# Optimization experiments

Measured on AMD Instinct MI355X. Metric: run time of the kernel, lower is better.

The kernel has to match this reference:

```python
import jax, jax.numpy as jnp
import numpy as np
from jax import lax

RADIUS = 0.3
NSAMPLE = 16
NPOINT = 1024
NH = 1   # num_heading_bin
NS = 18  # num_size_cluster
EPS = 1e-5  # torch BatchNorm eps


def _bn(x, g, b, m, v):
    # eval-mode batchnorm over the last (channel) axis
    return (x - m) * (g / jnp.sqrt(v + EPS)) + b


def _fps(xyz, npoint):
    # furthest point sampling; xyz: (B,K,3) -> (B,npoint) int32 indices
    B, K, _ = xyz.shape
    def body(carry, _):
        dists, far = carry
        cur = jnp.take_along_axis(xyz, far[:, None, None], axis=1)  # (B,1,3)
        d = jnp.sum((xyz - cur) ** 2, -1)                           # (B,K)
        dists = jnp.minimum(dists, d)
        nxt = jnp.argmax(dists, -1).astype(jnp.int32)
        return (dists, nxt), far
    init = (jnp.full((B, K), 1e10, xyz.dtype), jnp.zeros((B,), jnp.int32))
    _, inds = lax.scan(body, init, None, length=npoint)
    return jnp.swapaxes(inds, 0, 1)  # (B, npoint)


def _ball_query(xyz, new_xyz):
    # first-NSAMPLE points within RADIUS of each center, pad with first hit
    K = xyz.shape[1]
    d2 = jnp.sum((new_xyz[:, :, None, :] - xyz[:, None, :, :]) ** 2, -1)  # (B,S,K)
    mask = d2 < RADIUS ** 2
    idx = jnp.where(mask, jnp.arange(K, dtype=jnp.int32)[None, None, :], K)
    idx = jnp.sort(idx, -1)[..., :NSAMPLE]
    first = idx[..., :1]
    idx = jnp.where(idx == K, first, idx)
    idx = jnp.where(idx == K, 0, idx)  # degenerate: no neighbor at all
    return idx  # (B,S,NSAMPLE)


def setup_inputs() -> dict:
    key = jax.random.key(0)
    ks = jax.random.split(key, 32)
    inp = {}
    inp['xyz'] = jax.random.normal(ks[0], (8, 8192, 3), jnp.float32)
    inp['features'] = jax.random.normal(ks[1], (8, 256, 8192), jnp.float32)
    i = 2
    # shared MLP: 259 -> 128 -> 128 -> 128 (conv2d 1x1, no bias, then BN)
    for l, (o, c) in enumerate([(128, 259), (128, 128), (128, 128)]):
        inp[f'mlp_w{l}'] = jax.random.normal(ks[i], (o, c), jnp.float32) * 0.1; i += 1
        inp[f'mlp_g{l}'] = jnp.ones((o,), jnp.float32)
        inp[f'mlp_b{l}'] = jnp.zeros((o,), jnp.float32)
        inp[f'mlp_m{l}'] = jax.random.normal(ks[i], (o,), jnp.float32) * 0.01; i += 1
        inp[f'mlp_v{l}'] = jax.random.uniform(ks[i], (o,), jnp.float32, 0.5, 1.5); i += 1
    # box head convs (conv1d k=1)
    for nm, (o, c) in [('c1', (128, 128)), ('c2', (128, 128)), ('c3', (97, 128))]:
        inp[f'{nm}_w'] = jax.random.normal(ks[i], (o, c), jnp.float32) * 0.1; i += 1
        inp[f'{nm}_b'] = jnp.zeros((o,), jnp.float32)
    for nm in ['bn1', 'bn2']:
        inp[f'{nm}_g'] = jnp.ones((128,), jnp.float32)
        inp[f'{nm}_b'] = jnp.zeros((128,), jnp.float32)
        inp[f'{nm}_m'] = jax.random.normal(ks[i], (128,), jnp.float32) * 0.01; i += 1
        inp[f'{nm}_v'] = jax.random.uniform(ks[i], (128,), jnp.float32, 0.5, 1.5); i += 1
    inp['mean_size_arr'] = jax.random.uniform(ks[i], (NS, 3), jnp.float32, 0.3, 2.0)
    return inp


def reference(xyz, features,
              mlp_w0, mlp_g0, mlp_b0, mlp_m0, mlp_v0,
              mlp_w1, mlp_g1, mlp_b1, mlp_m1, mlp_v1,
              mlp_w2, mlp_g2, mlp_b2, mlp_m2, mlp_v2,
              c1_w, c1_b, bn1_g, bn1_b, bn1_m, bn1_v,
              c2_w, c2_b, bn2_g, bn2_b, bn2_m, bn2_v,
              c3_w, c3_b, mean_size_arr):
    B = xyz.shape[0]
    # --- vote aggregation: FPS + ball query + group + shared MLP + maxpool ---
    fps_inds = _fps(xyz, NPOINT)
    new_xyz = jnp.take_along_axis(xyz, fps_inds[..., None], axis=1)  # (B,S,3)
    idx = _ball_query(xyz, new_xyz)                                  # (B,S,n)
    gather = jax.vmap(lambda a, i: a[i])
    g_xyz = (gather(xyz, idx) - new_xyz[:, :, None, :]) / RADIUS     # normalize_xyz
    g_f = gather(jnp.swapaxes(features, 1, 2), idx)                  # (B,S,n,256)
    h = jnp.concatenate([g_xyz, g_f], -1)                            # (B,S,n,259)
    for w, g, b, m, v in ((mlp_w0, mlp_g0, mlp_b0, mlp_m0, mlp_v0),
                          (mlp_w1, mlp_g1, mlp_b1, mlp_m1, mlp_v1),
                          (mlp_w2, mlp_g2, mlp_b2, mlp_m2, mlp_v2)):
        h = jax.nn.relu(_bn(jnp.einsum('bsnc,oc->bsno', h, w), g, b, m, v))
    feat = jnp.max(h, axis=2)                                        # (B,S,128)
    # --- box head (conv1d k=1 == per-point linear) ---
    net = jax.nn.relu(_bn(jnp.einsum('bsc,oc->bso', feat, c1_w) + c1_b,
                          bn1_g, bn1_b, bn1_m, bn1_v))
    net = jax.nn.relu(_bn(jnp.einsum('bsc,oc->bso', net, c2_w) + c2_b,
                          bn2_g, bn2_b, bn2_m, bn2_v))
    net = jnp.einsum('bsc,oc->bso', net, c3_w) + c3_b                # (B,S,97)
    # --- decode_scores ---
    obj = net[..., 0:2]
    center = new_xyz + net[..., 2:5]
    hs = net[..., 5:5 + NH]
    hr = net[..., 5 + NH:5 + 2 * NH] * (np.pi / NH)
    ss = net[..., 5 + 2 * NH:5 + 2 * NH + NS]
    srn = net[..., 5 + 2 * NH + NS:5 + 2 * NH + 4 * NS].reshape(B, NPOINT, NS, 3)
    sr = (srn * mean_size_arr[None, None]).reshape(B, NPOINT, NS * 3)
    sem = net[..., 5 + 2 * NH + 4 * NS:]
    return jnp.concatenate([obj, center, hs, hr, ss, sr, sem], -1)   # (B,S,97)
```

## Files before the change

### kernel.cpp

```cpp
#include <hip/hip_runtime.h>
#include <cstdint>
#include <cstddef>

#define BATCH   8
#define KPTS    8192
#define NPT     1024
#define NSAMP   16
#define RAD2    0.09f

typedef float f32x2 __attribute__((ext_vector_type(2)));
typedef float f32x4 __attribute__((ext_vector_type(4)));
typedef short s16x4 __attribute__((ext_vector_type(4)));
typedef short s16x8 __attribute__((ext_vector_type(8)));

__device__ __forceinline__ unsigned short f2bf(float x) {
    unsigned u = __float_as_uint(x);
    return (unsigned short)((u + 0x7fffu + ((u >> 16) & 1u)) >> 16);
}

template <int CTRL>
__device__ __forceinline__ unsigned long long dpp_max_step(unsigned long long v) {
    unsigned int lo = (unsigned int)v, hi = (unsigned int)(v >> 32);
    unsigned int lo2 = (unsigned int)__builtin_amdgcn_update_dpp(0, (int)lo, CTRL, 0xf, 0xf, true);
    unsigned int hi2 = (unsigned int)__builtin_amdgcn_update_dpp(0, (int)hi, CTRL, 0xf, 0xf, true);
    unsigned long long o = ((unsigned long long)hi2 << 32) | lo2;
    return o > v ? o : v;
}

__global__ __launch_bounds__(512, 1) void fps_f0_kernel(
    const float* __restrict__ xyz, float* __restrict__ new_xyz,
    const float* __restrict__ feats, const float* __restrict__ w0,
    float* __restrict__ f0out) {
    __shared__ float xs[KPTS], ys[KPTS], zs[KPTS];
    __shared__ __align__(16) unsigned long long wslot[2][8];
    __shared__ int   hist[NPT];
    __shared__ float As[16 * 128];
    __shared__ float Bs[16 * 130];

    const int tid = threadIdx.x;

    if (blockIdx.x >= 8) {
        const int bid = blockIdx.x - 8;
        const int b   = bid >> 6;
        const int p0  = (bid & 63) << 7;
        const int rb  = (tid >> 4) << 2;
        const int ob  = tid & 15;
        const float* fb = feats + (size_t)b * 256 * KPTS;

        float acc[4][8];
#pragma unroll
        for (int r = 0; r < 4; ++r)
#pragma unroll
            for (int c = 0; c < 8; ++c) acc[r][c] = 0.f;

        for (int k0 = 0; k0 < 256; k0 += 16) {
#pragma unroll
            for (int i = 0; i < 4; ++i) {
                int e = tid + (i << 9);
                int kk = e >> 7, pc = e & 127;
                As[kk * 128 + pc] = fb[(size_t)(k0 + kk) * KPTS + p0 + pc];
            }
#pragma unroll
            for (int i = 0; i < 4; ++i) {
                int e = tid + (i << 9);
                int o = e >> 4, kk = e & 15;
                Bs[kk * 130 + o] = w0[o * 259 + 3 + k0 + kk];
            }
            __syncthreads();
#pragma unroll
            for (int kk = 0; kk < 16; ++kk) {
                float a[4], wvv[8];
#pragma unroll
                for (int r = 0; r < 4; ++r) a[r] = As[kk * 128 + rb + r];
#pragma unroll
                for (int c = 0; c < 8; ++c) wvv[c] = Bs[kk * 130 + ob + (c << 4)];
#pragma unroll
                for (int r = 0; r < 4; ++r)
#pragma unroll
                    for (int c = 0; c < 8; ++c) acc[r][c] = fmaf(a[r], wvv[c], acc[r][c]);
            }
            __syncthreads();
        }
#pragma unroll
        for (int r = 0; r < 4; ++r) {
            float* outp = f0out + ((size_t)b * KPTS + p0 + rb + r) * 128 + ob;
#pragma unroll
            for (int c = 0; c < 8; ++c) outp[c << 4] = acc[r][c];
        }
        return;
    }

    {
#pragma clang fp contract(off)
        const int b = blockIdx.x;
        const float* xb = xyz + (size_t)b * KPTS * 3;

        for (int i = tid; i < KPTS; i += 512) {
            xs[i] = xb[i * 3 + 0];
            ys[i] = xb[i * 3 + 1];
            zs[i] = xb[i * 3 + 2];
        }
        __syncthreads();

        const int base = tid << 4;
        f32x2 px[8], py[8], pz[8], dmn[8];
#pragma unroll
        for (int j = 0; j < 8; ++j) {
            int i0 = base + (j << 1);
            px[j] = (f32x2){xs[i0], xs[i0 + 1]};
            py[j] = (f32x2){ys[i0], ys[i0 + 1]};
            pz[j] = (f32x2){zs[i0], zs[i0 + 1]};
            dmn[j] = (f32x2){1e10f, 1e10f};
        }

        int far = 0;
        for (int it = 0; it < NPT; ++it) {
            if (tid == 0) hist[it] = far;
            const float cx = xs[far], cy = ys[far], cz = zs[far];
            const f32x2 cx2 = (f32x2){cx, cx};
            const f32x2 cy2 = (f32x2){cy, cy};
            const f32x2 cz2 = (f32x2){cz, cz};

            f32x2 mm = (f32x2){-1.0f, -1.0f};
#pragma unroll
            for (int j = 0; j < 8; ++j) {
                f32x2 dx = px[j] - cx2;
                f32x2 dy = py[j] - cy2;
                f32x2 dz = pz[j] - cz2;
                f32x2 d  = (dx * dx + dy * dy) + dz * dz;
                f32x2 nd = __builtin_elementwise_min(dmn[j], d);
                dmn[j] = nd;
                mm = __builtin_elementwise_max(mm, nd);
            }
            float lmax = fmaxf(mm.x, mm.y);

            int ci = 0x7fffffff;
#pragma unroll
            for (int j = 0; j < 8; ++j) {
                if (dmn[j].x == lmax) ci = min(ci, base + (j << 1));
                if (dmn[j].y == lmax) ci = min(ci, base + (j << 1) + 1);
            }

            unsigned long long pk =
                ((unsigned long long)__float_as_uint(lmax) << 32) | (unsigned)(8191 - ci);

            pk = dpp_max_step<0x111>(pk);
            pk = dpp_max_step<0x112>(pk);
            pk = dpp_max_step<0x114>(pk);
            pk = dpp_max_step<0x118>(pk);
            pk = dpp_max_step<0x142>(pk);
            pk = dpp_max_step<0x143>(pk);

            if ((tid & 63) == 63) wslot[it & 1][tid >> 6] = pk;
            __syncthreads();

            ulonglong2 s01 = *(const ulonglong2*)&wslot[it & 1][0];
            ulonglong2 s23 = *(const ulonglong2*)&wslot[it & 1][2];
            ulonglong2 s45 = *(const ulonglong2*)&wslot[it & 1][4];
            ulonglong2 s67 = *(const ulonglong2*)&wslot[it & 1][6];
            unsigned long long g = s01.x;
            if (s01.y > g) g = s01.y;
            if (s23.x > g) g = s23.x;
            if (s23.y > g) g = s23.y;
            if (s45.x > g) g = s45.x;
            if (s45.y > g) g = s45.y;
            if (s67.x > g) g = s67.x;
            if (s67.y > g) g = s67.y;
            far = 8191 - (int)(unsigned)(g & 0xffffffffull);
        }

        for (int i = tid; i < NPT; i += 512) {
            int idx = hist[i];
            float* o = new_xyz + ((size_t)b * NPT + i) * 3;
            o[0] = xs[idx]; o[1] = ys[idx]; o[2] = zs[idx];
        }
    }
}

__global__ __launch_bounds__(256) void ballq_kernel(const float* __restrict__ xyz,
                                                    const float* __restrict__ new_xyz,
                                                    int* __restrict__ idxout) {
    const int tid  = threadIdx.x;
    const int lane = tid & 63;
    const int q    = (blockIdx.x << 2) + (tid >> 6);
    const int b    = q >> 10;
    const float* xb = xyz + (size_t)b * KPTS * 3;
    const float qx = new_xyz[q * 3 + 0];
    const float qy = new_xyz[q * 3 + 1];
    const float qz = new_xyz[q * 3 + 2];
    int* op = idxout + q * NSAMP;

    int total = 0;
    int first_p = 0;
    for (int c = 0; c < KPTS / 64; ++c) {
        int p = (c << 6) + lane;
        float pxv = xb[p * 3 + 0], pyv = xb[p * 3 + 1], pzv = xb[p * 3 + 2];
        float dx = __fsub_rn(qx, pxv), dy = __fsub_rn(qy, pyv), dz = __fsub_rn(qz, pzv);
        float d2 = __fadd_rn(__fadd_rn(__fmul_rn(dx, dx), __fmul_rn(dy, dy)),
                             __fmul_rn(dz, dz));
        bool pred = d2 < RAD2;
        unsigned long long mask = __ballot(pred);
        if (total == 0 && mask != 0ull) first_p = (c << 6) + (int)__builtin_ctzll(mask);
        if (pred) {
            int rank = (int)__popcll(mask & ((1ull << lane) - 1ull));
            int slot = total + rank;
            if (slot < NSAMP) op[slot] = p;
        }
        total += (int)__popcll(mask);
        if (total >= NSAMP) break;
    }
    if (total < NSAMP && lane >= total && lane < NSAMP) op[lane] = first_p;
}

#define HB 136

__global__ __launch_bounds__(256) void mlp_kernel(
    const float* __restrict__ f0, const int* __restrict__ idxw,
    const float* __restrict__ xyz, const float* __restrict__ new_xyz,
    const float* __restrict__ w0,
    const float* __restrict__ g0, const float* __restrict__ b0,
    const float* __restrict__ m0, const float* __restrict__ v0,
    const float* __restrict__ w1,
    const float* __restrict__ g1, const float* __restrict__ b1a,
    const float* __restrict__ m1, const float* __restrict__ v1,
    const float* __restrict__ w2,
    const float* __restrict__ g2, const float* __restrict__ b2a,
    const float* __restrict__ m2, const float* __restrict__ v2,
    float* __restrict__ featout) {
    const int tid = threadIdx.x;
    const int q0  = blockIdx.x << 2;
    const int b   = q0 >> 10;

    __shared__ __align__(16) unsigned short hbf[64 * HB];
    __shared__ __align__(16) unsigned short Wsh[128 * HB];
    __shared__ float gx[64], gy[64], gz[64];
    __shared__ int   pidx[64];
    __shared__ float s0[128], t0[128], wxs[128], wys[128], wzs[128];
    __shared__ float s1[128], t1[128], s2[128], t2[128];

    if (tid < 64) pidx[tid] = idxw[(q0 + (tid >> 4)) * NSAMP + (tid & 15)];
    if (tid < 128) {
        float sc = g0[tid] / sqrtf(v0[tid] + 1e-5f);
        s0[tid] = sc; t0[tid] = b0[tid] - m0[tid] * sc;
        sc = g1[tid] / sqrtf(v1[tid] + 1e-5f);
        s1[tid] = sc; t1[tid] = b1a[tid] - m1[tid] * sc;
        sc = g2[tid] / sqrtf(v2[tid] + 1e-5f);
        s2[tid] = sc; t2[tid] = b2a[tid] - m2[tid] * sc;
        wxs[tid] = w0[tid * 259 + 0];
        wys[tid] = w0[tid * 259 + 1];
        wzs[tid] = w0[tid * 259 + 2];
    }
    __syncthreads();
    if (tid < 64) {
        int p = pidx[tid];
        int q = q0 + (tid >> 4);
        const float* pp = xyz + ((size_t)b * KPTS + p) * 3;
        const float* nq = new_xyz + (size_t)q * 3;
        gx[tid] = (pp[0] - nq[0]) / 0.3f;
        gy[tid] = (pp[1] - nq[1]) / 0.3f;
        gz[tid] = (pp[2] - nq[2]) / 0.3f;
    }
    __syncthreads();

#pragma unroll 2
    for (int i = 0; i < 8; ++i) {
        int e = tid + (i << 8);
        int row = e >> 5, o = (e & 31) << 2;
        int p = pidx[row];
        float4 v4 = *(const float4*)(f0 + ((size_t)b * KPTS + p) * 128 + o);
        float gxr = gx[row], gyr = gy[row], gzr = gz[row];
        float r0 = fmaf(wzs[o + 0], gzr, fmaf(wys[o + 0], gyr, fmaf(wxs[o + 0], gxr, v4.x)));
        float r1 = fmaf(wzs[o + 1], gzr, fmaf(wys[o + 1], gyr, fmaf(wxs[o + 1], gxr, v4.y)));
        float r2 = fmaf(wzs[o + 2], gzr, fmaf(wys[o + 2], gyr, fmaf(wxs[o + 2], gxr, v4.z)));
        float r3 = fmaf(wzs[o + 3], gzr, fmaf(wys[o + 3], gyr, fmaf(wxs[o + 3], gxr, v4.w)));
        s16x4 c4;
        c4.x = (short)f2bf(fmaxf(fmaf(r0, s0[o + 0], t0[o + 0]), 0.f));
        c4.y = (short)f2bf(fmaxf(fmaf(r1, s0[o + 1], t0[o + 1]), 0.f));
        c4.z = (short)f2bf(fmaxf(fmaf(r2, s0[o + 2], t0[o + 2]), 0.f));
        c4.w = (short)f2bf(fmaxf(fmaf(r3, s0[o + 3], t0[o + 3]), 0.f));
        *(s16x4*)&hbf[row * HB + o] = c4;
    }
#pragma unroll 4
    for (int i = 0; i < 16; ++i) {
        int e = tid + (i << 8);
        int o = e >> 5;
        int kt = (e & 31) << 2;
        float4 w4 = *(const float4*)(w1 + o * 128 + kt);
        s16x4 c4 = { (short)f2bf(w4.x), (short)f2bf(w4.y),
                     (short)f2bf(w4.z), (short)f2bf(w4.w) };
        *(s16x4*)&Wsh[o * HB + kt] = c4;
    }
    __syncthreads();

    const int w    = tid >> 6;
    const int lane = tid & 63;
    const int l15  = lane & 15;
    const int quad = lane >> 4;
    const int wrow = w << 4;

    f32x4 acc[8];
#pragma unroll
    for (int t = 0; t < 8; ++t) acc[t] = (f32x4){0.f, 0.f, 0.f, 0.f};
#pragma unroll
    for (int k0 = 0; k0 < 128; k0 += 32) {
        s16x8 a = *(const s16x8*)&hbf[(wrow + l15) * HB + k0 + (quad << 3)];
#pragma unroll
        for (int t = 0; t < 8; ++t) {
            s16x8 bf = *(const s16x8*)&Wsh[((t << 4) + l15) * HB + k0 + (quad << 3)];
            acc[t] = __builtin_amdgcn_mfma_f32_16x16x32_bf16(a, bf, acc[t], 0, 0, 0);
        }
    }
    __syncthreads();

#pragma unroll
    for (int t = 0; t < 8; ++t) {
        int o = (t << 4) + l15;
        float ss = s1[o], tt = t1[o];
#pragma unroll
        for (int r = 0; r < 4; ++r) {
            float v = fmaxf(fmaf(acc[t][r], ss, tt), 0.f);
            hbf[(wrow + (quad << 2) + r) * HB + o] = f2bf(v);
        }
    }
#pragma unroll 4
    for (int i = 0; i < 16; ++i) {
        int e = tid + (i << 8);
        int o = e >> 5;
        int kt = (e & 31) << 2;
        float4 w4 = *(const float4*)(w2 + o * 128 + kt);
        s16x4 c4 = { (short)f2bf(w4.x), (short)f2bf(w4.y),
                     (short)f2bf(w4.z), (short)f2bf(w4.w) };
        *(s16x4*)&Wsh[o * HB + kt] = c4;
    }
    __syncthreads();

#pragma unroll
    for (int t = 0; t < 8; ++t) acc[t] = (f32x4){0.f, 0.f, 0.f, 0.f};
#pragma unroll
    for (int k0 = 0; k0 < 128; k0 += 32) {
        s16x8 a = *(const s16x8*)&hbf[(wrow + l15) * HB + k0 + (quad << 3)];
#pragma unroll
        for (int t = 0; t < 8; ++t) {
            s16x8 bf = *(const s16x8*)&Wsh[((t << 4) + l15) * HB + k0 + (quad << 3)];
            acc[t] = __builtin_amdgcn_mfma_f32_16x16x32_bf16(a, bf, acc[t], 0, 0, 0);
        }
    }

#pragma unroll
    for (int t = 0; t < 8; ++t) {
        int o = (t << 4) + l15;
        float ss = s2[o], tt = t2[o];
        float m0v = fmaxf(fmaf(acc[t][0], ss, tt), 0.f);
        float m1v = fmaxf(fmaf(acc[t][1], ss, tt), 0.f);
        float m2v = fmaxf(fmaf(acc[t][2], ss, tt), 0.f);
        float m3v = fmaxf(fmaf(acc[t][3], ss, tt), 0.f);
        float m = fmaxf(fmaxf(m0v, m1v), fmaxf(m2v, m3v));
        m = fmaxf(m, __shfl_xor(m, 16));
        m = fmaxf(m, __shfl_xor(m, 32));
        if (quad == 0)
            featout[(size_t)(q0 + w) * 128 + o] = m;
    }
}

__global__ __launch_bounds__(256) void head_kernel(
    const float* __restrict__ feat, const float* __restrict__ new_xyz,
    const float* __restrict__ c1w, const float* __restrict__ c1b,
    const float* __restrict__ c2w, const float* __restrict__ c2b,
    const float* __restrict__ c3w, const float* __restrict__ c3b,
    const float* __restrict__ bg1, const float* __restrict__ bb1,
    const float* __restrict__ bm1, const float* __restrict__ bv1,
    const float* __restrict__ bg2, const float* __restrict__ bb2,
    const float* __restrict__ bm2, const float* __restrict__ bv2,
    const float* __restrict__ msz, float* __restrict__ out) {
    const int tid = threadIdx.x;
    const int q0  = blockIdx.x << 3;
    __shared__ float fs[8][128], n1[8][128], n2[8][128];
    __shared__ float s1[128], t1[128], s2[128], t2[128], ms[54];

#pragma unroll
    for (int i = 0; i < 4; ++i) {
        int e = tid + (i << 8);
        fs[e >> 7][e & 127] = feat[(size_t)q0 * 128 + e];
    }
    if (tid < 128) {
        float sc = bg1[tid] / sqrtf(bv1[tid] + 1e-5f);
        s1[tid] = sc; t1[tid] = bb1[tid] - bm1[tid] * sc;
        sc = bg2[tid] / sqrtf(bv2[tid] + 1e-5f);
        s2[tid] = sc; t2[tid] = bb2[tid] - bm2[tid] * sc;
    }
    if (tid < 54) ms[tid] = msz[tid];
    __syncthreads();

    const int o    = tid & 127;
    const int half = tid >> 7;

    {
        float a[4];
#pragma unroll
        for (int j = 0; j < 4; ++j) a[j] = c1b[o];
        const float* wr = c1w + o * 128;
        for (int k = 0; k < 128; k += 4) {
            float4 w4 = *(const float4*)(wr + k);
#pragma unroll
            for (int j = 0; j < 4; ++j) {
                int qq = half * 4 + j;
                a[j] = fmaf(fs[qq][k + 0], w4.x, a[j]);
                a[j] = fmaf(fs[qq][k + 1], w4.y, a[j]);
                a[j] = fmaf(fs[qq][k + 2], w4.z, a[j]);
                a[j] = fmaf(fs[qq][k + 3], w4.w, a[j]);
            }
        }
#pragma unroll
        for (int j = 0; j < 4; ++j)
            n1[half * 4 + j][o] = fmaxf(fmaf(a[j], s1[o], t1[o]), 0.f);
    }
    __syncthreads();
    {
        float a[4];
#pragma unroll
        for (int j = 0; j < 4; ++j) a[j] = c2b[o];
        const float* wr = c2w + o * 128;
        for (int k = 0; k < 128; k += 4) {
            float4 w4 = *(const float4*)(wr + k);
#pragma unroll
            for (int j = 0; j < 4; ++j) {
                int qq = half * 4 + j;
                a[j] = fmaf(n1[qq][k + 0], w4.x, a[j]);
                a[j] = fmaf(n1[qq][k + 1], w4.y, a[j]);
                a[j] = fmaf(n1[qq][k + 2], w4.z, a[j]);
                a[j] = fmaf(n1[qq][k + 3], w4.w, a[j]);
            }
        }
#pragma unroll
        for (int j = 0; j < 4; ++j)
            n2[half * 4 + j][o] = fmaxf(fmaf(a[j], s2[o], t2[o]), 0.f);
    }
    __syncthreads();
    if (o < 97) {
        float a[4];
#pragma unroll
        for (int j = 0; j < 4; ++j) a[j] = c3b[o];
        const float* wr = c3w + o * 128;
        for (int k = 0; k < 128; k += 4) {
            float4 w4 = *(const float4*)(wr + k);
#pragma unroll
            for (int j = 0; j < 4; ++j) {
                int qq = half * 4 + j;
                a[j] = fmaf(n2[qq][k + 0], w4.x, a[j]);
                a[j] = fmaf(n2[qq][k + 1], w4.y, a[j]);
                a[j] = fmaf(n2[qq][k + 2], w4.z, a[j]);
                a[j] = fmaf(n2[qq][k + 3], w4.w, a[j]);
            }
        }
#pragma unroll
        for (int j = 0; j < 4; ++j) {
            int q = q0 + half * 4 + j;
            float v = a[j];
            if (o >= 2 && o < 5) v += new_xyz[(size_t)q * 3 + (o - 2)];
            else if (o == 6) v *= 3.14159265358979323846f;
            else if (o >= 25 && o < 79) v *= ms[o - 25];
            out[(size_t)q * 97 + o] = v;
        }
    }
}

extern "C" void kernel_launch(void* const* d_in, const int* in_sizes, int n_in,
                              void* d_out, int out_size, void* d_ws, size_t ws_size,
                              hipStream_t stream) {
    const float* xyz      = (const float*)d_in[0];
    const float* features = (const float*)d_in[1];
    const float* w0  = (const float*)d_in[2];
    const float* g0  = (const float*)d_in[3];
    const float* b0  = (const float*)d_in[4];
    const float* m0  = (const float*)d_in[5];
    const float* v0  = (const float*)d_in[6];
    const float* w1  = (const float*)d_in[7];
    const float* g1  = (const float*)d_in[8];
    const float* b1  = (const float*)d_in[9];
    const float* m1  = (const float*)d_in[10];
    const float* v1  = (const float*)d_in[11];
    const float* w2  = (const float*)d_in[12];
    const float* g2  = (const float*)d_in[13];
    const float* b2  = (const float*)d_in[14];
    const float* m2  = (const float*)d_in[15];
    const float* v2  = (const float*)d_in[16];
    const float* c1w = (const float*)d_in[17];
    const float* c1b = (const float*)d_in[18];
    const float* c2w = (const float*)d_in[19];
    const float* c2b = (const float*)d_in[20];
    const float* c3w = (const float*)d_in[21];
    const float* c3b = (const float*)d_in[22];
    const float* bg1 = (const float*)d_in[23];
    const float* bb1 = (const float*)d_in[24];
    const float* bm1 = (const float*)d_in[25];
    const float* bv1 = (const float*)d_in[26];
    const float* bg2 = (const float*)d_in[27];
    const float* bb2 = (const float*)d_in[28];
    const float* bm2 = (const float*)d_in[29];
    const float* bv2 = (const float*)d_in[30];
    const float* msz = (const float*)d_in[31];

    float* F0   = (float*)d_ws;
    float* feat = F0 + (size_t)BATCH * KPTS * 128;
    int*   idxw = (int*)(feat + (size_t)BATCH * NPT * 128);
    float* nxyz = (float*)(idxw + (size_t)BATCH * NPT * NSAMP);
    float* outp = (float*)d_out;

    fps_f0_kernel<<<8 + BATCH * (KPTS / 128), 512, 0, stream>>>(
        xyz, nxyz, features, w0, F0);
    ballq_kernel<<<BATCH * NPT / 4, 256, 0, stream>>>(xyz, nxyz, idxw);
    mlp_kernel  <<<BATCH * NPT / 4, 256, 0, stream>>>(
        F0, idxw, xyz, nxyz, w0, g0, b0, m0, v0,
        w1, g1, b1, m1, v1, w2, g2, b2, m2, v2, feat);
    head_kernel <<<BATCH * NPT / 8, 256, 0, stream>>>(
        feat, nxyz, c1w, c1b, c2w, c2b, c3w, c3b,
        bg1, bb1, bm1, bv1, bg2, bb2, bm2, bv2, msz, outp);
}
```

Before: 1.252 ms.

## Fuse ball query, grouped MLP and box head into one tail kernel

After: 1.567 ms. 1.25x slower.

```diff
diff --git a/kernel.cpp b/kernel.cpp
--- a/kernel.cpp
+++ b/kernel.cpp
@@ -177,46 +177,11 @@
     }
 }
 
-__global__ __launch_bounds__(256) void ballq_kernel(const float* __restrict__ xyz,
-                                                    const float* __restrict__ new_xyz,
-                                                    int* __restrict__ idxout) {
-    const int tid  = threadIdx.x;
-    const int lane = tid & 63;
-    const int q    = (blockIdx.x << 2) + (tid >> 6);
-    const int b    = q >> 10;
-    const float* xb = xyz + (size_t)b * KPTS * 3;
-    const float qx = new_xyz[q * 3 + 0];
-    const float qy = new_xyz[q * 3 + 1];
-    const float qz = new_xyz[q * 3 + 2];
-    int* op = idxout + q * NSAMP;
-
-    int total = 0;
-    int first_p = 0;
-    for (int c = 0; c < KPTS / 64; ++c) {
-        int p = (c << 6) + lane;
-        float pxv = xb[p * 3 + 0], pyv = xb[p * 3 + 1], pzv = xb[p * 3 + 2];
-        float dx = __fsub_rn(qx, pxv), dy = __fsub_rn(qy, pyv), dz = __fsub_rn(qz, pzv);
-        float d2 = __fadd_rn(__fadd_rn(__fmul_rn(dx, dx), __fmul_rn(dy, dy)),
-                             __fmul_rn(dz, dz));
-        bool pred = d2 < RAD2;
-        unsigned long long mask = __ballot(pred);
-        if (total == 0 && mask != 0ull) first_p = (c << 6) + (int)__builtin_ctzll(mask);
-        if (pred) {
-            int rank = (int)__popcll(mask & ((1ull << lane) - 1ull));
-            int slot = total + rank;
-            if (slot < NSAMP) op[slot] = p;
-        }
-        total += (int)__popcll(mask);
-        if (total >= NSAMP) break;
-    }
-    if (total < NSAMP && lane >= total && lane < NSAMP) op[lane] = first_p;
-}
-
 #define HB 136
 
-__global__ __launch_bounds__(256) void mlp_kernel(
-    const float* __restrict__ f0, const int* __restrict__ idxw,
-    const float* __restrict__ xyz, const float* __restrict__ new_xyz,
+__global__ __launch_bounds__(256) void tail_kernel(
+    const float* __restrict__ f0, const float* __restrict__ xyz,
+    const float* __restrict__ new_xyz,
     const float* __restrict__ w0,
     const float* __restrict__ g0, const float* __restrict__ b0,
     const float* __restrict__ m0, const float* __restrict__ v0,
@@ -226,7 +191,14 @@
     const float* __restrict__ w2,
     const float* __restrict__ g2, const float* __restrict__ b2a,
     const float* __restrict__ m2, const float* __restrict__ v2,
-    float* __restrict__ featout) {
+    const float* __restrict__ c1w, const float* __restrict__ c1b,
+    const float* __restrict__ c2w, const float* __restrict__ c2b,
+    const float* __restrict__ c3w, const float* __restrict__ c3b,
+    const float* __restrict__ bg1, const float* __restrict__ bb1,
+    const float* __restrict__ bm1, const float* __restrict__ bv1,
+    const float* __restrict__ bg2, const float* __restrict__ bb2,
+    const float* __restrict__ bm2, const float* __restrict__ bv2,
+    const float* __restrict__ msz, float* __restrict__ out) {
     const int tid = threadIdx.x;
     const int q0  = blockIdx.x << 2;
     const int b   = q0 >> 10;
@@ -237,8 +209,9 @@
     __shared__ int   pidx[64];
     __shared__ float s0[128], t0[128], wxs[128], wys[128], wzs[128];
     __shared__ float s1[128], t1[128], s2[128], t2[128];
-
-    if (tid < 64) pidx[tid] = idxw[(q0 + (tid >> 4)) * NSAMP + (tid & 15)];
+    __shared__ float hs1[128], ht1[128], hs2[128], ht2[128], ms[54];
+    __shared__ float featL[4][128], n1[4][128], n2[4][128];
+
     if (tid < 128) {
         float sc = g0[tid] / sqrtf(v0[tid] + 1e-5f);
         s0[tid] = sc; t0[tid] = b0[tid] - m0[tid] * sc;
@@ -246,11 +219,49 @@
         s1[tid] = sc; t1[tid] = b1a[tid] - m1[tid] * sc;
         sc = g2[tid] / sqrtf(v2[tid] + 1e-5f);
         s2[tid] = sc; t2[tid] = b2a[tid] - m2[tid] * sc;
+        sc = bg1[tid] / sqrtf(bv1[tid] + 1e-5f);
+        hs1[tid] = sc; ht1[tid] = bb1[tid] - bm1[tid] * sc;
+        sc = bg2[tid] / sqrtf(bv2[tid] + 1e-5f);
+        hs2[tid] = sc; ht2[tid] = bb2[tid] - bm2[tid] * sc;
         wxs[tid] = w0[tid * 259 + 0];
         wys[tid] = w0[tid * 259 + 1];
         wzs[tid] = w0[tid * 259 + 2];
     }
-    __syncthreads();
+    if (tid < 54) ms[tid] = msz[tid];
+
+    {
+        const int w    = tid >> 6;
+        const int lane = tid & 63;
+        const int q    = q0 + w;
+        const float* xb = xyz + (size_t)b * KPTS * 3;
+        const float qx = new_xyz[q * 3 + 0];
+        const float qy = new_xyz[q * 3 + 1];
+        const float qz = new_xyz[q * 3 + 2];
+        int* op = &pidx[w * NSAMP];
+
+        int total = 0;
+        int first_p = 0;
+        for (int c = 0; c < KPTS / 64; ++c) {
+            int p = (c << 6) + lane;
+            float pxv = xb[p * 3 + 0], pyv = xb[p * 3 + 1], pzv = xb[p * 3 + 2];
+            float dx = __fsub_rn(qx, pxv), dy = __fsub_rn(qy, pyv), dz = __fsub_rn(qz, pzv);
+            float d2 = __fadd_rn(__fadd_rn(__fmul_rn(dx, dx), __fmul_rn(dy, dy)),
+                                 __fmul_rn(dz, dz));
+            bool pred = d2 < RAD2;
+            unsigned long long mask = __ballot(pred);
+            if (total == 0 && mask != 0ull) first_p = (c << 6) + (int)__builtin_ctzll(mask);
+            if (pred) {
+                int rank = (int)__popcll(mask & ((1ull << lane) - 1ull));
+                int slot = total + rank;
+                if (slot < NSAMP) op[slot] = p;
+            }
+            total += (int)__popcll(mask);
+            if (total >= NSAMP) break;
+        }
+        if (total < NSAMP && lane >= total && lane < NSAMP) op[lane] = first_p;
+    }
+    __syncthreads();
+
     if (tid < 64) {
         int p = pidx[tid];
         int q = q0 + (tid >> 4);
@@ -345,7 +356,6 @@
             acc[t] = __builtin_amdgcn_mfma_f32_16x16x32_bf16(a, bf, acc[t], 0, 0, 0);
         }
     }
-
 #pragma unroll
     for (int t = 0; t < 8; ++t) {
         int o = (t << 4) + l15;
@@ -357,109 +367,78 @@
         float m = fmaxf(fmaxf(m0v, m1v), fmaxf(m2v, m3v));
         m = fmaxf(m, __shfl_xor(m, 16));
         m = fmaxf(m, __shfl_xor(m, 32));
-        if (quad == 0)
-            featout[(size_t)(q0 + w) * 128 + o] = m;
-    }
-}
-
-__global__ __launch_bounds__(256) void head_kernel(
-    const float* __restrict__ feat, const float* __restrict__ new_xyz,
-    const float* __restrict__ c1w, const float* __restrict__ c1b,
-    const float* __restrict__ c2w, const float* __restrict__ c2b,
-    const float* __restrict__ c3w, const float* __restrict__ c3b,
-    const float* __restrict__ bg1, const float* __restrict__ bb1,
-    const float* __restrict__ bm1, const float* __restrict__ bv1,
-    const float* __restrict__ bg2, const float* __restrict__ bb2,
-    const float* __restrict__ bm2, const float* __restrict__ bv2,
-    const float* __restrict__ msz, float* __restrict__ out) {
-    const int tid = threadIdx.x;
-    const int q0  = blockIdx.x << 3;
-    __shared__ float fs[8][128], n1[8][128], n2[8][128];
-    __shared__ float s1[128], t1[128], s2[128], t2[128], ms[54];
-
-#pragma unroll
-    for (int i = 0; i < 4; ++i) {
-        int e = tid + (i << 8);
-        fs[e >> 7][e & 127] = feat[(size_t)q0 * 128 + e];
-    }
-    if (tid < 128) {
-        float sc = bg1[tid] / sqrtf(bv1[tid] + 1e-5f);
-        s1[tid] = sc; t1[tid] = bb1[tid] - bm1[tid] * sc;
-        sc = bg2[tid] / sqrtf(bv2[tid] + 1e-5f);
-        s2[tid] = sc; t2[tid] = bb2[tid] - bm2[tid] * sc;
-    }
-    if (tid < 54) ms[tid] = msz[tid];
-    __syncthreads();
-
-    const int o    = tid & 127;
-    const int half = tid >> 7;
+        if (quad == 0) featL[w][o] = m;
+    }
+    __syncthreads();
 
     {
-        float a[4];
-#pragma unroll
-        for (int j = 0; j < 4; ++j) a[j] = c1b[o];
-        const float* wr = c1w + o * 128;
-        for (int k = 0; k < 128; k += 4) {
-            float4 w4 = *(const float4*)(wr + k);
-#pragma unroll
-            for (int j = 0; j < 4; ++j) {
-                int qq = half * 4 + j;
-                a[j] = fmaf(fs[qq][k + 0], w4.x, a[j]);
-                a[j] = fmaf(fs[qq][k + 1], w4.y, a[j]);
-                a[j] = fmaf(fs[qq][k + 2], w4.z, a[j]);
-                a[j] = fmaf(fs[qq][k + 3], w4.w, a[j]);
-            }
-        }
-#pragma unroll
-        for (int j = 0; j < 4; ++j)
-            n1[half * 4 + j][o] = fmaxf(fmaf(a[j], s1[o], t1[o]), 0.f);
-    }
-    __syncthreads();
-    {
-        float a[4];
-#pragma unroll
-        for (int j = 0; j < 4; ++j) a[j] = c2b[o];
-        const float* wr = c2w + o * 128;
-        for (int k = 0; k < 128; k += 4) {
-            float4 w4 = *(const float4*)(wr + k);
-#pragma unroll
-            for (int j = 0; j < 4; ++j) {
-                int qq = half * 4 + j;
-                a[j] = fmaf(n1[qq][k + 0], w4.x, a[j]);
-                a[j] = fmaf(n1[qq][k + 1], w4.y, a[j]);
-                a[j] = fmaf(n1[qq][k + 2], w4.z, a[j]);
-                a[j] = fmaf(n1[qq][k + 3], w4.w, a[j]);
-            }
-        }
-#pragma unroll
-        for (int j = 0; j < 4; ++j)
-            n2[half * 4 + j][o] = fmaxf(fmaf(a[j], s2[o], t2[o]), 0.f);
-    }
-    __syncthreads();
-    if (o < 97) {
-        float a[4];
-#pragma unroll
-        for (int j = 0; j < 4; ++j) a[j] = c3b[o];
-        const float* wr = c3w + o * 128;
-        for (int k = 0; k < 128; k += 4) {
-            float4 w4 = *(const float4*)(wr + k);
-#pragma unroll
-            for (int j = 0; j < 4; ++j) {
-                int qq = half * 4 + j;
-                a[j] = fmaf(n2[qq][k + 0], w4.x, a[j]);
-                a[j] = fmaf(n2[qq][k + 1], w4.y, a[j]);
-                a[j] = fmaf(n2[qq][k + 2], w4.z, a[j]);
-                a[j] = fmaf(n2[qq][k + 3], w4.w, a[j]);
-            }
-        }
-#pragma unroll
-        for (int j = 0; j < 4; ++j) {
-            int q = q0 + half * 4 + j;
-            float v = a[j];
-            if (o >= 2 && o < 5) v += new_xyz[(size_t)q * 3 + (o - 2)];
-            else if (o == 6) v *= 3.14159265358979323846f;
-            else if (o >= 25 && o < 79) v *= ms[o - 25];
-            out[(size_t)q * 97 + o] = v;
+        const int o    = tid & 127;
+        const int half = tid >> 7;
+
+        {
+            float a[2];
+            a[0] = c1b[o]; a[1] = c1b[o];
+            const float* wr = c1w + o * 128;
+            for (int k = 0; k < 128; k += 4) {
+                float4 w4 = *(const float4*)(wr + k);
+#pragma unroll
+                for (int j = 0; j < 2; ++j) {
+                    int qq = half * 2 + j;
+                    a[j] = fmaf(featL[qq][k + 0], w4.x, a[j]);
+                    a[j] = fmaf(featL[qq][k + 1], w4.y, a[j]);
+                    a[j] = fmaf(featL[qq][k + 2], w4.z, a[j]);
+                    a[j] = fmaf(featL[qq][k + 3], w4.w, a[j]);
+                }
+            }
+#pragma unroll
+            for (int j = 0; j < 2; ++j)
+                n1[half * 2 + j][o] = fmaxf(fmaf(a[j], hs1[o], ht1[o]), 0.f);
+        }
+        __syncthreads();
+        {
+            float a[2];
+            a[0] = c2b[o]; a[1] = c2b[o];
+            const float* wr = c2w + o * 128;
+            for (int k = 0; k < 128; k += 4) {
+                float4 w4 = *(const float4*)(wr + k);
+#pragma unroll
+                for (int j = 0; j < 2; ++j) {
+                    int qq = half * 2 + j;
+                    a[j] = fmaf(n1[qq][k + 0], w4.x, a[j]);
+                    a[j] = fmaf(n1[qq][k + 1], w4.y, a[j]);
+                    a[j] = fmaf(n1[qq][k + 2], w4.z, a[j]);
+                    a[j] = fmaf(n1[qq][k + 3], w4.w, a[j]);
+                }
+            }
+#pragma unroll
+            for (int j = 0; j < 2; ++j)
+                n2[half * 2 + j][o] = fmaxf(fmaf(a[j], hs2[o], ht2[o]), 0.f);
+        }
+        __syncthreads();
+        if (o < 97) {
+            float a[2];
+            a[0] = c3b[o]; a[1] = c3b[o];
+            const float* wr = c3w + o * 128;
+            for (int k = 0; k < 128; k += 4) {
+                float4 w4 = *(const float4*)(wr + k);
+#pragma unroll
+                for (int j = 0; j < 2; ++j) {
+                    int qq = half * 2 + j;
+                    a[j] = fmaf(n2[qq][k + 0], w4.x, a[j]);
+                    a[j] = fmaf(n2[qq][k + 1], w4.y, a[j]);
+                    a[j] = fmaf(n2[qq][k + 2], w4.z, a[j]);
+                    a[j] = fmaf(n2[qq][k + 3], w4.w, a[j]);
+                }
+            }
+#pragma unroll
+            for (int j = 0; j < 2; ++j) {
+                int q = q0 + half * 2 + j;
+                float v = a[j];
+                if (o >= 2 && o < 5) v += new_xyz[(size_t)q * 3 + (o - 2)];
+                else if (o == 6) v *= 3.14159265358979323846f;
+                else if (o >= 25 && o < 79) v *= ms[o - 25];
+                out[(size_t)q * 97 + o] = v;
+            }
         }
     }
 }
@@ -501,18 +480,14 @@
     const float* msz = (const float*)d_in[31];
 
     float* F0   = (float*)d_ws;
-    float* feat = F0 + (size_t)BATCH * KPTS * 128;
-    int*   idxw = (int*)(feat + (size_t)BATCH * NPT * 128);
-    float* nxyz = (float*)(idxw + (size_t)BATCH * NPT * NSAMP);
+    float* nxyz = F0 + (size_t)BATCH * KPTS * 128;
     float* outp = (float*)d_out;
 
     fps_f0_kernel<<<8 + BATCH * (KPTS / 128), 512, 0, stream>>>(
         xyz, nxyz, features, w0, F0);
-    ballq_kernel<<<BATCH * NPT / 4, 256, 0, stream>>>(xyz, nxyz, idxw);
-    mlp_kernel  <<<BATCH * NPT / 4, 256, 0, stream>>>(
-        F0, idxw, xyz, nxyz, w0, g0, b0, m0, v0,
-        w1, g1, b1, m1, v1, w2, g2, b2, m2, v2, feat);
-    head_kernel <<<BATCH * NPT / 8, 256, 0, stream>>>(
-        feat, nxyz, c1w, c1b, c2w, c2b, c3w, c3b,
+    tail_kernel<<<BATCH * NPT / 4, 256, 0, stream>>>(
+        F0, xyz, nxyz, w0, g0, b0, m0, v0,
+        w1, g1, b1, m1, v1, w2, g2, b2, m2, v2,
+        c1w, c1b, c2w, c2b, c3w, c3b,
         bg1, bb1, bm1, bv1, bg2, bb2, bm2, bv2, msz, outp);
 }
```
